# Optimization experiments

Hardware: AMD Instinct MI355X
Metric: run time of the kernel (lower is better)

## Reference

```python
import jax, jax.numpy as jnp
import numpy as np

TOLX = 1e-12
TOLFUN = 1e-06
MAXITER = 1000
ALPHA = 1e-4
MIN_LAMBDA = 0.1
MAX_LAMBDA = 0.5
MAX_STEPS = 10  # fixed unroll budget; Newton converges in < 10 iterations for this problem
BS, NY = 200000, 8


def setup_inputs():
    key = jax.random.key(0)
    k1, k2, k3 = jax.random.split(key, 3)
    y0 = jax.random.normal(k1, (BS, NY), dtype=jnp.float32)
    W = 0.1 * jax.random.normal(k2, (NY, NY), dtype=jnp.float32)
    V = 0.1 * jax.random.normal(k3, (NY, NY), dtype=jnp.float32)
    dt = jnp.asarray(0.1, dtype=jnp.float32)
    t = jnp.asarray(1.0, dtype=jnp.float32)
    return {"y0": y0, "dt": dt, "t": t, "W": W, "V": V}


def _safe_div(n, d, eps=1e-30):
    ok = jnp.abs(d) > eps
    return jnp.where(ok, n / jnp.where(ok, d, 1.0), 0.0)


def _solver(y0, dt, t, W, V):
    bs, ny = y0.shape
    one = jnp.float32(1.0)

    def delta_S(tt, y):
        # test ODE right-hand side g(t, y): mildly nonlinear, acts per-sample
        return jnp.tanh(y @ W) @ V - 0.1 * y + 0.01 * jnp.sin(tt)

    def err(y):  # implicit-Euler residual, (bs, ny)
        return (y - y0) / dt - delta_S(t, y)

    def _err_single(yb, y0b):
        return (yb - y0b) / dt - (jnp.tanh(yb @ W) @ V - 0.1 * yb + 0.01 * jnp.sin(t))

    def batched_jac(y):
        # (bs, ny, ny): d err_b / d y_b; matches torch batch-diagonal of autograd jacobian
        return jax.vmap(jax.jacfwd(_err_single), in_axes=(0, 0))(y, y0)

    F0 = err(y0)
    jac0 = batched_jac(y0)
    rn0 = jnp.max(jnp.abs(F0), axis=1)
    fobj0 = jnp.einsum('bi,bi->b', F0, F0)

    state0 = dict(y=y0, yold=y0, F=F0, dy=jnp.zeros_like(y0), jac=jac0,
                  resnorm=rn0, resnorm0=100.0 * rn0,
                  lam=one, lam1=one, lam2=jnp.float32(0.5),
                  fold=fobj0, f2=fobj0, slope=jnp.zeros((bs,), y0.dtype),
                  lam_min=jnp.float32(0.0), niter=jnp.int32(0), exitflag=jnp.int32(1))

    def body(s, _):
        active = (((jnp.max(s['resnorm']) > TOLFUN) | (s['lam'] < 1.0))
                  & (s['exitflag'] >= 0) & (s['niter'] <= MAXITER))

        # --- lam == 1: fresh Newton direction, slope, objective ---
        is_newton = s['lam'] == 1.0
        recompute = jnp.max(_safe_div(s['resnorm'], s['resnorm0'])) > 0.2
        fresh_jac = batched_jac(s['y'])
        jac = jnp.where(is_newton & recompute, fresh_jac, s['jac'])
        dy_n = -jnp.linalg.solve(jac, s['F'][..., None])[..., 0]  # lstsq on square == solve
        gvec = jnp.einsum('bi,bij->bj', s['F'], jac)
        slope_n = jnp.einsum('bj,bj->b', gvec, dy_n)
        fold_n = jnp.einsum('bi,bi->b', s['F'], s['F'])
        lam_min_n = _safe_div(jnp.float32(TOLX),
                              jnp.max(jnp.abs(dy_n) / jnp.maximum(jnp.abs(s['y']), 1.0)))

        dy = jnp.where(is_newton, dy_n, s['dy'])
        slope = jnp.where(is_newton, slope_n, s['slope'])
        fold = jnp.where(is_newton, fold_n, s['fold'])
        yold = jnp.where(is_newton, s['y'], s['yold'])
        lam_min = jnp.where(is_newton, lam_min_n, s['lam_min'])
        niter = jnp.where(is_newton, s['niter'] + 1, s['niter'])

        brk = s['lam'] < lam_min            # -> exitflag = 2, freeze state
        bad = ~jnp.all(jnp.isfinite(dy))    # -> exitflag = -1, freeze state

        # --- trial step + trust-region line search ---
        lam = s['lam']
        y_new = yold + dy * lam
        F_new = err(y_new)
        f_obj = jnp.einsum('bi,bi->b', F_new, F_new)
        lam1 = lam
        lam2, f2 = s['lam2'], s['f2']

        backtrack = jnp.any(f_obj > fold + ALPHA * lam * slope)
        # quadratic model (first backtrack)
        lam_quad = jnp.min(_safe_div(-slope / 2.0, f_obj - fold - slope))
        # cubic model (subsequent backtracks)
        A = _safe_div(one, lam1 - lam2)
        inv1 = _safe_div(one, lam1 * lam1)
        inv2 = _safe_div(one, lam2 * lam2)
        B = jnp.stack([jnp.stack([inv1, -inv2]), jnp.stack([-lam2 * inv1, lam1 * inv2])])
        C = jnp.stack([f_obj - fold - lam1 * slope, f2 - fold - lam2 * slope])  # (2, bs)
        ab = A * (B @ C)
        a, b = ab[0], ab[1]
        disc = b * b - 3.0 * a * slope
        sq = jnp.sqrt(jnp.maximum(disc, 0.0))
        lam_tmp = jnp.where(jnp.all(a == 0.0), _safe_div(-slope, 2.0 * b),
                   jnp.where(jnp.any(disc < 0.0), MAX_LAMBDA * lam1,
                    jnp.where(jnp.any(b <= 0.0), _safe_div(-b + sq, 3.0 * a),
                     _safe_div(-slope, b + sq))))
        lam_cubic = jnp.min(jnp.minimum(lam_tmp, MAX_LAMBDA * lam1))
        lam_bt = jnp.where(lam == 1.0, lam_quad, lam_cubic)
        nanf = ~jnp.all(jnp.isfinite(f_obj))
        lam_new = jnp.where(backtrack, lam_bt, jnp.where(nanf, MAX_LAMBDA * lam1, one))

        cont = lam_new < 1.0  # retry with smaller lambda next iteration (the `continue` path)
        lam2_new = jnp.where(cont, lam1, lam2)
        f2_new = jnp.where(cont, f_obj, f2)
        lam_new = jnp.where(cont, jnp.maximum(lam_new, MIN_LAMBDA * lam1), lam_new)
        resnorm_new = jnp.where(cont, s['resnorm'], jnp.max(jnp.abs(F_new), axis=1))
        resnorm0_new = jnp.where(cont, s['resnorm0'], s['resnorm'])

        upd = active & (~brk) & (~bad)
        exitflag = jnp.where(active & brk, jnp.int32(2),
                    jnp.where(active & (~brk) & bad, jnp.int32(-1), s['exitflag']))
        sel = lambda new, old: jnp.where(upd, new, old)

        ns = dict(y=sel(y_new, s['y']), yold=sel(yold, s['yold']), F=sel(F_new, s['F']),
                  dy=sel(dy, s['dy']), jac=sel(jac, s['jac']),
                  resnorm=sel(resnorm_new, s['resnorm']), resnorm0=sel(resnorm0_new, s['resnorm0']),
                  lam=sel(lam_new, s['lam']), lam1=sel(lam1, s['lam1']), lam2=sel(lam2_new, s['lam2']),
                  fold=sel(fold, s['fold']), f2=sel(f2_new, s['f2']), slope=sel(slope, s['slope']),
                  lam_min=sel(lam_min, s['lam_min']),
                  niter=jnp.where(active, niter, s['niter']), exitflag=exitflag)
        return ns, None

    sN, _ = jax.lax.scan(body, state0, None, length=MAX_STEPS)
    return sN['y'], sN['F'], sN['exitflag']


def reference(y0, dt, t, W, V):
    y, F, exitflag = _solver(y0, dt, t, W, V)
    return (y, F, exitflag)
```

## Files before the change

kernel.cpp:

```cpp
#include <hip/hip_runtime.h>
#include <hip/hip_cooperative_groups.h>

namespace cg = cooperative_groups;

#define BSZ 200000
#define NSTEPS 10
#define TOLFUN_C 1e-6f
#define ALPHA_C 1e-4f

#define CNTHR 256
#define CNBLK 512
#define CNT   (CNBLK*CNTHR)
#define SPT   2
#define SLOTS (CNTHR*SPT)

#define FNTHR 256
#define FNBLK ((BSZ + FNTHR - 1)/FNTHR)

#define OFF_Y     ((size_t)0)
#define OFF_YOLD  ((size_t)BSZ*8)
#define OFF_DY    ((size_t)BSZ*16)
#define OFF_SJ    ((size_t)BSZ*24)
#define OFF_FOLD  ((size_t)BSZ*32)
#define OFF_SLOPE ((size_t)BSZ*33)
#define OFF_RESN  ((size_t)BSZ*34)
#define OFF_F2    ((size_t)BSZ*35)
#define OFF_TFO   ((size_t)BSZ*36)
#define OFF_TRN   ((size_t)BSZ*37)
#define OFF_R     ((size_t)BSZ*38)

#define RSTRIDE 64
#define NSLOT   9
#define R_TOT   (2 + NSTEPS*NSLOT)
#define KEY_MAX_IDENT 0x007FFFFFu
#define KEY_MIN_IDENT 0xFF800000u

static __device__ __forceinline__ float nanmax2(float a, float b){
    return (__builtin_isnan(a) || __builtin_isnan(b)) ? __builtin_nanf("") : fmaxf(a, b);
}
static __device__ __forceinline__ float nanmin2(float a, float b){
    return (__builtin_isnan(a) || __builtin_isnan(b)) ? __builtin_nanf("") : fminf(a, b);
}
static __device__ __forceinline__ float safe_div(float n, float d){
    return (fabsf(d) > 1e-30f) ? (n / d) : 0.0f;
}
static __device__ __forceinline__ unsigned fkey(float x){
    unsigned u = __float_as_uint(x);
    return (u & 0x80000000u) ? ~u : (u | 0x80000000u);
}
static __device__ __forceinline__ float funkey(unsigned u){
    return (u & 0x80000000u) ? __uint_as_float(u & 0x7FFFFFFFu) : __uint_as_float(~u);
}
static __device__ __forceinline__ unsigned fkey_max(float x){
    if (__builtin_isnan(x)) x = __uint_as_float(0x7FC00000u);
    return fkey(x);
}
static __device__ __forceinline__ unsigned fkey_min(float x){
    if (__builtin_isnan(x)) x = __uint_as_float(0xFFC00000u);
    return fkey(x);
}
static __device__ __forceinline__ void ld8(const float* p, float* v){
    float4 a = ((const float4*)p)[0], b = ((const float4*)p)[1];
    v[0]=a.x; v[1]=a.y; v[2]=a.z; v[3]=a.w; v[4]=b.x; v[5]=b.y; v[6]=b.z; v[7]=b.w;
}
static __device__ __forceinline__ void st8(float* p, const float* v){
    float4 a, b;
    a.x=v[0]; a.y=v[1]; a.z=v[2]; a.w=v[3];
    b.x=v[4]; b.y=v[5]; b.z=v[6]; b.w=v[7];
    ((float4*)p)[0]=a; ((float4*)p)[1]=b;
}
static __device__ __forceinline__ unsigned ldslot(const unsigned* p){
    return __hip_atomic_load(p, __ATOMIC_RELAXED, __HIP_MEMORY_SCOPE_AGENT);
}
static __device__ __forceinline__ void stslot(unsigned* p, unsigned v){
    __hip_atomic_store(p, v, __ATOMIC_RELAXED, __HIP_MEMORY_SCOPE_AGENT);
}

static __device__ __forceinline__ void computeFz(
    const float* yv, const float* y0v, float dt, float c0,
    const float* sW, const float* sV, float* Fo, float* zo)
{
    float u[8];
    #pragma unroll
    for (int k=0;k<8;k++){
        float acc = 0.f;
        #pragma unroll
        for (int m=0;m<8;m++) acc += yv[m]*sW[m*8+k];
        u[k]=acc;
    }
    #pragma unroll
    for (int k=0;k<8;k++) zo[k] = tanhf(u[k]);
    #pragma unroll
    for (int i=0;i<8;i++){
        float tv = 0.f;
        #pragma unroll
        for (int k=0;k<8;k++) tv += zo[k]*sV[k*8+i];
        Fo[i] = (yv[i]-y0v[i])/dt - ((tv - 0.1f*yv[i]) + c0);
    }
}

static __device__ __forceinline__ void devInit2(const float* y0v,
    float* yold, float* dy, float* sj, float* F_out,
    float& fold_o, float& slope_o, float& resn_o, float& f2_o,
    float dt, float c0, const float* sW, const float* sV,
    float& rn_red, float& rat_red)
{
    #pragma unroll
    for (int i=0;i<8;i++){ yold[i]=y0v[i]; dy[i]=0.f; }
    float z[8];
    computeFz(y0v, y0v, dt, c0, sW, sV, F_out, z);
    #pragma unroll
    for (int k=0;k<8;k++) sj[k] = 1.0f - z[k]*z[k];
    float fold = 0.f;
    #pragma unroll
    for (int i=0;i<8;i++) fold += F_out[i]*F_out[i];
    float rn0 = fabsf(F_out[0]);
    #pragma unroll
    for (int i=1;i<8;i++) rn0 = nanmax2(rn0, fabsf(F_out[i]));
    fold_o=fold; slope_o=0.f; resn_o=rn0; f2_o=fold;
    rn_red  = nanmax2(rn_red, rn0);
    rat_red = nanmax2(rat_red, safe_div(rn0, 100.0f*rn0));
}

static __device__ __forceinline__ void devA4(const float* y_cur, const float* Fv,
    float* yold, float* dy, float* sj, float& fold_o, float& slope_o,
    float invdt, const float* sW, const float* sV,
    bool recompute, float& gml, bool& nf)
{
    if (recompute){
        float u[8];
        #pragma unroll
        for (int k=0;k<8;k++){
            float acc = 0.f;
            #pragma unroll
            for (int m=0;m<8;m++) acc += y_cur[m]*sW[m*8+k];
            u[k]=acc;
        }
        #pragma unroll
        for (int k=0;k<8;k++){ float z = tanhf(u[k]); sj[k] = 1.0f - z*z; }
    }
    const float c  = invdt + 0.1f;
    const float rc = 1.0f / c;
    float s[8], acc[8];
    #pragma unroll
    for (int i=0;i<8;i++){ s[i]=Fv[i]; acc[i]=Fv[i]; }
    for (int it=0; it<7; ++it){
        float w1[8];
        #pragma unroll
        for (int k=0;k<8;k++){
            float a = 0.f;
            #pragma unroll
            for (int j=0;j<8;j++) a += sW[j*8+k]*s[j];
            w1[k] = a*sj[k];
        }
        #pragma unroll
        for (int i=0;i<8;i++){
            float a = 0.f;
            #pragma unroll
            for (int k=0;k<8;k++) a += sV[k*8+i]*w1[k];
            s[i] = a*rc;
            acc[i] += s[i];
        }
    }
    #pragma unroll
    for (int i=0;i<8;i++) dy[i] = -(rc*acc[i]);
    float vf[8];
    #pragma unroll
    for (int k=0;k<8;k++){
        float a = 0.f;
        #pragma unroll
        for (int i=0;i<8;i++) a += sV[k*8+i]*Fv[i];
        vf[k] = a*sj[k];
    }
    float fold = 0.f, slope = 0.f;
    #pragma unroll
    for (int i=0;i<8;i++) fold += Fv[i]*Fv[i];
    #pragma unroll
    for (int j=0;j<8;j++){
        float a = 0.f;
        #pragma unroll
        for (int k=0;k<8;k++) a += sW[j*8+k]*vf[k];
        float gvj = c*Fv[j] - a;
        slope += gvj*dy[j];
    }
    #pragma unroll
    for (int i=0;i<8;i++){
        yold[i] = y_cur[i];
        float rr = fabsf(dy[i]) / nanmax2(fabsf(y_cur[i]), 1.0f);
        gml = nanmax2(gml, rr);
        nf = nf || !__builtin_isfinite(dy[i]);
    }
    fold_o = fold; slope_o = slope;
}

static __device__ __forceinline__ void devA2(const float* y_cur, const float* y0v,
    float* yold, float* dy, float* sj, float& fold_o, float& slope_o,
    float dt, float invdt, float c0, const float* sW, const float* sV,
    bool recompute, float& gml, bool& nf)
{
    float Fv[8], z[8];
    computeFz(y_cur, y0v, dt, c0, sW, sV, Fv, z);
    if (recompute){
        #pragma unroll
        for (int k=0;k<8;k++) sj[k] = 1.0f - z[k]*z[k];
    }
    devA4(y_cur, Fv, yold, dy, sj, fold_o, slope_o, invdt, sW, sV, false, gml, nf);
}

static __device__ __forceinline__ void devB2(const float* yold, const float* dy,
    const float* y0v, float foldv, float slopev, float resnv, float f2v,
    float dt, float c0, const float* sW, const float* sV, float lam, float lam2v,
    float* Ft, float& tfo_o, float& trn_o,
    bool& armijo, float& lq, bool& aNot0, bool& dN, bool& ble,
    float& mX, float& mZ, float& mW, bool& nanf, float& trnR, float& ratR)
{
    float yn[8];
    #pragma unroll
    for (int i=0;i<8;i++) yn[i] = yold[i] + dy[i]*lam;
    float z[8];
    computeFz(yn, y0v, dt, c0, sW, sV, Ft, z);
    float f_obj = 0.f;
    #pragma unroll
    for (int i=0;i<8;i++) f_obj += Ft[i]*Ft[i];
    float rn = fabsf(Ft[0]);
    #pragma unroll
    for (int i=1;i<8;i++) rn = nanmax2(rn, fabsf(Ft[i]));
    tfo_o = f_obj; trn_o = rn;
    armijo = armijo || (f_obj > (foldv + (ALPHA_C*lam)*slopev));
    lq = nanmin2(lq, safe_div((-slopev)*0.5f, (f_obj - foldv) - slopev));
    float lam1v = lam;
    float Af = safe_div(1.0f, lam1v - lam2v);
    float i1 = safe_div(1.0f, lam1v*lam1v);
    float i2 = safe_div(1.0f, lam2v*lam2v);
    float Cc0 = (f_obj - foldv) - lam1v*slopev;
    float Cc1 = (f2v   - foldv) - lam2v*slopev;
    float av = Af*(i1*Cc0 - i2*Cc1);
    float bv = Af*((-(lam2v*i1))*Cc0 + (lam1v*i2)*Cc1);
    float disc = bv*bv - (3.0f*av)*slopev;
    float dm = __builtin_isnan(disc) ? disc : fmaxf(disc, 0.0f);
    float sq = sqrtf(dm);
    aNot0 = aNot0 || (av != 0.0f);
    dN    = dN    || (disc < 0.0f);
    ble   = ble   || (bv <= 0.0f);
    mX = nanmin2(mX, safe_div(-slopev, 2.0f*bv));
    mZ = nanmin2(mZ, safe_div(-bv + sq, 3.0f*av));
    mW = nanmin2(mW, safe_div(-slopev, bv + sq));
    nanf = nanf || !__builtin_isfinite(f_obj);
    trnR = nanmax2(trnR, rn);
    ratR = nanmax2(ratR, safe_div(rn, resnv));
}

struct ScalarState {
    float lam, lam1, lam2, lam_min, maxrn, ratmax;
    int   niter, exitflag;
    bool  upd_prev, cont_prev;
};

static __device__ void advance(ScalarState& s, const unsigned* R, int j){
    const unsigned* r = R + (size_t)(2 + j*NSLOT)*RSTRIDE;
    unsigned v0 = ldslot(r + (size_t)0*RSTRIDE);
    unsigned v1 = ldslot(r + (size_t)1*RSTRIDE);
    unsigned v2 = ldslot(r + (size_t)2*RSTRIDE);
    unsigned v3 = ldslot(r + (size_t)3*RSTRIDE);
    unsigned v4 = ldslot(r + (size_t)4*RSTRIDE);
    unsigned v5 = ldslot(r + (size_t)5*RSTRIDE);
    unsigned v6 = ldslot(r + (size_t)6*RSTRIDE);
    unsigned v7 = ldslot(r + (size_t)7*RSTRIDE);
    unsigned v8 = ldslot(r + (size_t)8*RSTRIDE);
    bool active    = ((s.maxrn > TOLFUN_C) || (s.lam < 1.0f)) && (s.exitflag >= 0) && (s.niter <= 1000);
    bool is_newton = (s.lam == 1.0f);
    float lam_min_new = is_newton ? safe_div(1e-12f, funkey(v0)) : s.lam_min;
    bool brk = (s.lam < lam_min_new);
    bool bad = is_newton ? (v1 != 0u) : false;
    bool upd = active && !brk && !bad;
    int niter_new = active ? (is_newton ? s.niter + 1 : s.niter) : s.niter;
    int ef_new = s.exitflag;
    if (active && brk) ef_new = 2;
    else if (active && !brk && bad) ef_new = -1;
    bool cont = false;
    if (upd){
        float lam1c = s.lam;
        unsigned bm = v8;
        bool backtrack = (bm & 1u) != 0u;
        float lamq  = funkey(v2);
        bool allA0  = (bm & 2u) == 0u;
        bool anyDN  = (bm & 4u) != 0u;
        bool anyB0  = (bm & 8u) != 0u;
        float lam_tmp_min = allA0 ? funkey(v3)
                          : (anyDN ? (0.5f*lam1c)
                          : (anyB0 ? funkey(v4) : funkey(v5)));
        float lam_cubic = nanmin2(lam_tmp_min, 0.5f*lam1c);
        float lam_bt = (s.lam == 1.0f) ? lamq : lam_cubic;
        bool nanf = (bm & 16u) != 0u;
        float lam_new = backtrack ? lam_bt : (nanf ? 0.5f*lam1c : 1.0f);
        cont = (lam_new < 1.0f);
        float lam2_new = cont ? lam1c : s.lam2;
        if (cont) lam_new = nanmax2(lam_new, 0.1f*lam1c);
        float maxrn_new  = cont ? s.maxrn  : funkey(v6);
        float ratmax_new = cont ? s.ratmax : funkey(v7);
        s.lam = lam_new; s.lam1 = lam1c; s.lam2 = lam2_new;
        s.lam_min = lam_min_new; s.maxrn = maxrn_new; s.ratmax = ratmax_new;
    }
    s.niter = niter_new; s.exitflag = ef_new;
    s.upd_prev = upd; s.cont_prev = cont;
}

static __device__ ScalarState replayN(const unsigned* R, int n){
    ScalarState s;
    s.lam=1.0f; s.lam1=1.0f; s.lam2=0.5f; s.lam_min=0.0f;
    s.maxrn  = funkey(ldslot(&R[0]));
    s.ratmax = funkey(ldslot(&R[(size_t)1*RSTRIDE]));
    s.niter=0; s.exitflag=1; s.upd_prev=false; s.cont_prev=false;
    for (int j=0;j<n;++j) advance(s, R, j);
    return s;
}

__global__ __launch_bounds__(CNTHR, 2) void kFused(
    const float* __restrict__ y0g, const float* __restrict__ Wm, const float* __restrict__ Vm,
    const float* __restrict__ dtp, const float* __restrict__ tp,
    float* __restrict__ ws, float* __restrict__ out)
{
    cg::grid_group gridg = cg::this_grid();
    __shared__ float sW[64], sV[64];
    __shared__ float sSJ[8*SLOTS];
    __shared__ float sF0[8*SLOTS];
    __shared__ float sF1[8*SLOTS];
    __shared__ float redF[6][4];
    __shared__ unsigned redB[4];
    int t = threadIdx.x;
    if (t < 64) sW[t] = Wm[t];
    else if (t < 128) sV[t-64] = Vm[t-64];
    unsigned* R = (unsigned*)(ws + OFF_R);
    if (blockIdx.x == 0 && t < R_TOT){
        unsigned v;
        if (t < 2) v = KEY_MAX_IDENT;
        else {
            int off = (t - 2) % NSLOT;
            bool ismin = (off==2 || off==3 || off==4 || off==5);
            bool ismax = (off==0 || off==6 || off==7);
            v = ismin ? KEY_MIN_IDENT : (ismax ? KEY_MAX_IDENT : 0u);
        }
        stslot(&R[(size_t)t*RSTRIDE], v);
    }
    __syncthreads();
    gridg.sync();

    int gtid = blockIdx.x*CNTHR + t;
    float dt = *dtp, invdt = 1.0f/dt, c0 = 0.01f*sinf(*tp);

    bool  valid[SPT];
    float yold[SPT][8], dyv[SPT][8];
    float foldv[SPT], slopev[SPT], resnv[SPT], f2v[SPT], tfov[SPT], trnv[SPT];
    float lamc = 0.0f;
    int   pcur = 0;

    float rn_red = -__builtin_inff(), rat_red = -__builtin_inff();
    #pragma unroll
    for (int q=0;q<SPT;q++){
        int sid = gtid + q*CNT;
        int slot = q*CNTHR + t;
        valid[q] = sid < BSZ;
        if (valid[q]){
            float y0v[8], sjl[8], Fl[8];
            ld8(y0g + (size_t)sid*8, y0v);
            devInit2(y0v, yold[q], dyv[q], sjl, Fl,
                     foldv[q], slopev[q], resnv[q], f2v[q],
                     dt, c0, sW, sV, rn_red, rat_red);
            #pragma unroll
            for (int i=0;i<8;i++){ sSJ[i*SLOTS + slot] = sjl[i]; sF0[i*SLOTS + slot] = Fl[i]; }
            tfov[q]=0.f; trnv[q]=0.f;
        } else {
            #pragma unroll
            for (int i=0;i<8;i++){ sSJ[i*SLOTS + slot]=0; sF0[i*SLOTS + slot]=0; sF1[i*SLOTS + slot]=0;
                                   yold[q][i]=0; dyv[q][i]=0; }
            foldv[q]=0; slopev[q]=0; resnv[q]=0; f2v[q]=0; tfov[q]=0; trnv[q]=0;
        }
    }
    #pragma unroll
    for (int o=32;o>=1;o>>=1){
        rn_red  = nanmax2(rn_red,  __shfl_xor(rn_red,  o, 64));
        rat_red = nanmax2(rat_red, __shfl_xor(rat_red, o, 64));
    }
    {
        int w = t >> 6;
        if ((t & 63) == 0){ redF[0][w] = rn_red; redF[1][w] = rat_red; }
        __syncthreads();
        if (t == 0){
            float a = redF[0][0];
            #pragma unroll
            for (int w2=1;w2<4;w2++) a = nanmax2(a, redF[0][w2]);
            atomicMax(&R[0], fkey_max(a));
        } else if (t == 1){
            float b = redF[1][0];
            #pragma unroll
            for (int w2=1;w2<4;w2++) b = nanmax2(b, redF[1][w2]);
            atomicMax(&R[(size_t)1*RSTRIDE], fkey_max(b));
        }
    }
    gridg.sync();

    ScalarState S;
    S.lam=1.0f; S.lam1=1.0f; S.lam2=0.5f; S.lam_min=0.0f;
    S.maxrn  = funkey(ldslot(&R[0]));
    S.ratmax = funkey(ldslot(&R[(size_t)1*RSTRIDE]));
    S.niter=0; S.exitflag=1; S.upd_prev=false; S.cont_prev=false;

    #pragma unroll 1
    for (int k=1; k<=NSTEPS; ++k){
        if (S.upd_prev){
            lamc = S.lam1;
            pcur ^= 1;
            #pragma unroll
            for (int q=0;q<SPT;q++){
                if (!valid[q]) continue;
                if (S.cont_prev) f2v[q]  = tfov[q];
                else             resnv[q] = trnv[q];
            }
        }
        float* sFcur  = pcur ? sF1 : sF0;
        float* sFpend = pcur ? sF0 : sF1;
        bool active    = ((S.maxrn > TOLFUN_C) || (S.lam < 1.0f)) && (S.exitflag >= 0) && (S.niter <= 1000);
        bool is_newton = (S.lam == 1.0f);
        unsigned* r = R + (size_t)(2 + (k-1)*NSLOT)*RSTRIDE;

        if (active && is_newton){
            bool recompute = (S.ratmax > 0.2f);
            float gml = -__builtin_inff(); bool nf = false;
            #pragma unroll
            for (int q=0;q<SPT;q++){
                if (!valid[q]) continue;
                int slot = q*CNTHR + t;
                float y_cur[8], sjl[8], Fl[8];
                #pragma unroll
                for (int i=0;i<8;i++){
                    y_cur[i] = yold[q][i] + dyv[q][i]*lamc;
                    sjl[i]   = sSJ[i*SLOTS + slot];
                    Fl[i]    = sFcur[i*SLOTS + slot];
                }
                devA4(y_cur, Fl, yold[q], dyv[q], sjl, foldv[q], slopev[q],
                      invdt, sW, sV, recompute, gml, nf);
                if (recompute){
                    #pragma unroll
                    for (int i=0;i<8;i++) sSJ[i*SLOTS + slot] = sjl[i];
                }
            }
            lamc = 0.0f;
            #pragma unroll
            for (int o=32;o>=1;o>>=1) gml = nanmax2(gml, __shfl_xor(gml, o, 64));
            unsigned long long anym = __ballot(nf ? 1 : 0);
            int w = t >> 6;
            if ((t & 63) == 0){ redF[0][w] = gml; redB[w] = anym ? 1u : 0u; }
            __syncthreads();
            if (t == 0){
                float v = redF[0][0];
                #pragma unroll
                for (int w2=1;w2<4;w2++) v = nanmax2(v, redF[0][w2]);
                atomicMax(&r[0], fkey_max(v));
            } else if (t == 1){
                unsigned bm = redB[0]|redB[1]|redB[2]|redB[3];
                if (bm) atomicOr(&r[(size_t)1*RSTRIDE], 1u);
            }
            __syncthreads();
        }

        if (active){
            float lam = S.lam, lam2v = S.lam2;
            bool armijo=false, aNot0=false, dN=false, ble=false, nanf=false;
            float lq=__builtin_inff(), mX=__builtin_inff(), mZ=__builtin_inff(), mW=__builtin_inff();
            float trnR=-__builtin_inff(), ratR=-__builtin_inff();
            #pragma unroll
            for (int q=0;q<SPT;q++){
                if (!valid[q]) continue;
                int sid = gtid + q*CNT;
                int slot = q*CNTHR + t;
                float y0v[8], Ftl[8];
                ld8(y0g + (size_t)sid*8, y0v);
                devB2(yold[q], dyv[q], y0v, foldv[q], slopev[q], resnv[q], f2v[q],
                      dt, c0, sW, sV, lam, lam2v, Ftl, tfov[q], trnv[q],
                      armijo, lq, aNot0, dN, ble, mX, mZ, mW, nanf, trnR, ratR);
                #pragma unroll
                for (int i=0;i<8;i++) sFpend[i*SLOTS + slot] = Ftl[i];
            }
            #pragma unroll
            for (int o=32;o>=1;o>>=1){
                lq   = nanmin2(lq,   __shfl_xor(lq,   o, 64));
                mX   = nanmin2(mX,   __shfl_xor(mX,   o, 64));
                mZ   = nanmin2(mZ,   __shfl_xor(mZ,   o, 64));
                mW   = nanmin2(mW,   __shfl_xor(mW,   o, 64));
                trnR = nanmax2(trnR, __shfl_xor(trnR, o, 64));
                ratR = nanmax2(ratR, __shfl_xor(ratR, o, 64));
            }
            unsigned long long bArm = __ballot(armijo ? 1 : 0);
            unsigned long long bA0  = __ballot(aNot0  ? 1 : 0);
            unsigned long long bDN  = __ballot(dN     ? 1 : 0);
            unsigned long long bB0  = __ballot(ble    ? 1 : 0);
            unsigned long long bNF  = __ballot(nanf   ? 1 : 0);
            int w = t >> 6;
            if ((t & 63) == 0){
                redF[0][w]=lq; redF[1][w]=mX; redF[2][w]=mZ; redF[3][w]=mW;
                redF[4][w]=trnR; redF[5][w]=ratR;
                redB[w] = (bArm?1u:0u) | (bA0?2u:0u) | (bDN?4u:0u) | (bB0?8u:0u) | (bNF?16u:0u);
            }
            __syncthreads();
            if (t < 6){
                float v = redF[t][0];
                bool ismin = (t < 4);
                #pragma unroll
                for (int w2=1;w2<4;w2++) v = ismin ? nanmin2(v, redF[t][w2]) : nanmax2(v, redF[t][w2]);
                unsigned* p = &r[(size_t)(t + 2)*RSTRIDE];
                if (ismin) atomicMin(p, fkey_min(v));
                else       atomicMax(p, fkey_max(v));
            } else if (t == 6){
                unsigned bm = redB[0]|redB[1]|redB[2]|redB[3];
                if (bm) atomicOr(&r[(size_t)8*RSTRIDE], bm);
            }
        }

        gridg.sync();
        advance(S, R, k-1);
    }

    if (S.upd_prev){ lamc = S.lam1; pcur ^= 1; }
    float* sFout = pcur ? sF1 : sF0;
    #pragma unroll
    for (int q=0;q<SPT;q++){
        if (!valid[q]) continue;
        int sid = gtid + q*CNT;
        int slot = q*CNTHR + t;
        float yf[8], Fl[8];
        #pragma unroll
        for (int i=0;i<8;i++){
            yf[i] = yold[q][i] + dyv[q][i]*lamc;
            Fl[i] = sFout[i*SLOTS + slot];
        }
        st8(out + (size_t)sid*8, yf);
        st8(out + (size_t)BSZ*8 + (size_t)sid*8, Fl);
    }
    if (gtid == 0) out[(size_t)BSZ*16] = (float)S.exitflag;
}

__global__ void kPre(unsigned* __restrict__ R){
    int i = threadIdx.x;
    if (i >= R_TOT) return;
    unsigned v;
    if (i < 2) v = KEY_MAX_IDENT;
    else {
        int off = (i - 2) % NSLOT;
        bool ismin = (off==2 || off==3 || off==4 || off==5);
        bool ismax = (off==0 || off==6 || off==7);
        v = ismin ? KEY_MIN_IDENT : (ismax ? KEY_MAX_IDENT : 0u);
    }
    R[(size_t)i*RSTRIDE] = v;
}

__global__ __launch_bounds__(FNTHR) void fInit(
    const float* __restrict__ y0g, const float* __restrict__ Wm, const float* __restrict__ Vm,
    const float* __restrict__ dtp, const float* __restrict__ tp, float* __restrict__ ws)
{
    __shared__ float sW[64], sV[64];
    __shared__ float red[2][4];
    int t = threadIdx.x;
    if (t < 64) sW[t] = Wm[t];
    else if (t < 128) sV[t-64] = Vm[t-64];
    __syncthreads();
    unsigned* R = (unsigned*)(ws + OFF_R);
    int tid = blockIdx.x*FNTHR + t;
    bool valid = tid < BSZ;
    float dt = *dtp, c0 = 0.01f*sinf(*tp);
    float rn_red = -__builtin_inff(), rat_red = -__builtin_inff();
    if (valid){
        float y0v[8], yo[8], dv[8], sj[8], Fv[8], fold, slope, resn, f2;
        ld8(y0g + (size_t)tid*8, y0v);
        devInit2(y0v, yo, dv, sj, Fv, fold, slope, resn, f2, dt, c0, sW, sV, rn_red, rat_red);
        st8(ws+OFF_Y   +(size_t)tid*8, y0v);
        st8(ws+OFF_YOLD+(size_t)tid*8, yo);
        st8(ws+OFF_DY  +(size_t)tid*8, dv);
        st8(ws+OFF_SJ  +(size_t)tid*8, sj);
        ws[OFF_FOLD+tid]=fold; ws[OFF_SLOPE+tid]=slope;
        ws[OFF_RESN+tid]=resn; ws[OFF_F2+tid]=f2;
        ws[OFF_TFO+tid]=0.f;   ws[OFF_TRN+tid]=0.f;
    }
    #pragma unroll
    for (int o=32;o>=1;o>>=1){
        rn_red  = nanmax2(rn_red,  __shfl_xor(rn_red,  o, 64));
        rat_red = nanmax2(rat_red, __shfl_xor(rat_red, o, 64));
    }
    int w = t >> 6;
    if ((t & 63) == 0){ red[0][w]=rn_red; red[1][w]=rat_red; }
    __syncthreads();
    if (t == 0){
        float a = red[0][0];
        for (int w2=1;w2<4;w2++) a = nanmax2(a, red[0][w2]);
        atomicMax(&R[0], fkey_max(a));
    } else if (t == 1){
        float b = red[1][0];
        for (int w2=1;w2<4;w2++) b = nanmax2(b, red[1][w2]);
        atomicMax(&R[(size_t)1*RSTRIDE], fkey_max(b));
    }
}

__global__ __launch_bounds__(FNTHR) void fStep(
    const float* __restrict__ y0g, const float* __restrict__ Wm, const float* __restrict__ Vm,
    const float* __restrict__ dtp, const float* __restrict__ tp,
    float* __restrict__ ws, int step)
{
    __shared__ float sW[64], sV[64];
    __shared__ float redF[6][4];
    __shared__ unsigned redB[4];
    int t = threadIdx.x;
    if (t < 64) sW[t] = Wm[t];
    else if (t < 128) sV[t-64] = Vm[t-64];
    __syncthreads();
    unsigned* R = (unsigned*)(ws + OFF_R);
    ScalarState S = replayN(R, step-1);
    bool active    = ((S.maxrn > TOLFUN_C) || (S.lam < 1.0f)) && (S.exitflag >= 0) && (S.niter <= 1000);
    bool is_newton = (S.lam == 1.0f);
    if (!S.upd_prev && !active) return;

    int tid = blockIdx.x*FNTHR + t;
    bool valid = tid < BSZ;
    float dt = *dtp, invdt = 1.0f/dt, c0 = 0.01f*sinf(*tp);
    unsigned* r = R + (size_t)(2 + (step-1)*NSLOT)*RSTRIDE;

    float y0v[8], yv[8], yo[8], dv[8], sj[8], fold=0, slope=0, resn=0, f2=0;
    if (valid){
        ld8(y0g + (size_t)tid*8, y0v);
        ld8(ws+OFF_Y   +(size_t)tid*8, yv);
        ld8(ws+OFF_YOLD+(size_t)tid*8, yo);
        ld8(ws+OFF_DY  +(size_t)tid*8, dv);
        ld8(ws+OFF_SJ  +(size_t)tid*8, sj);
        fold=ws[OFF_FOLD+tid]; slope=ws[OFF_SLOPE+tid];
        resn=ws[OFF_RESN+tid]; f2=ws[OFF_F2+tid];
        if (S.upd_prev){
            #pragma unroll
            for (int i=0;i<8;i++) yv[i] = yo[i] + dv[i]*S.lam1;
            st8(ws+OFF_Y+(size_t)tid*8, yv);
            if (S.cont_prev){ f2 = ws[OFF_TFO+tid];  ws[OFF_F2+tid]   = f2; }
            else            { resn = ws[OFF_TRN+tid]; ws[OFF_RESN+tid] = resn; }
        }
    }
    if (!active) return;

    if (is_newton){
        bool recompute = (S.ratmax > 0.2f);
        float gml = -__builtin_inff(); bool nf = false;
        if (valid){
            devA2(yv, y0v, yo, dv, sj, fold, slope, dt, invdt, c0, sW, sV, recompute, gml, nf);
            st8(ws+OFF_YOLD+(size_t)tid*8, yo);
            st8(ws+OFF_DY  +(size_t)tid*8, dv);
            if (recompute) st8(ws+OFF_SJ+(size_t)tid*8, sj);
            ws[OFF_FOLD+tid]  = fold;
            ws[OFF_SLOPE+tid] = slope;
        }
        #pragma unroll
        for (int o=32;o>=1;o>>=1) gml = nanmax2(gml, __shfl_xor(gml, o, 64));
        unsigned long long anym = __ballot(nf ? 1 : 0);
        int w = t >> 6;
        if ((t & 63) == 0){ redF[0][w] = gml; redB[w] = anym ? 1u : 0u; }
        __syncthreads();
        if (t == 0){
            float v = redF[0][0];
            for (int w2=1;w2<4;w2++) v = nanmax2(v, redF[0][w2]);
            atomicMax(&r[0], fkey_max(v));
        } else if (t == 1){
            unsigned bm = redB[0]|redB[1]|redB[2]|redB[3];
            if (bm) atomicOr(&r[(size_t)1*RSTRIDE], 1u);
        }
        __syncthreads();
    }

    {
        float lam = S.lam, lam2v = S.lam2;
        bool armijo=false, aNot0=false, dN=false, ble=false, nanf=false;
        float lq=__builtin_inff(), mX=__builtin_inff(), mZ=__builtin_inff(), mW=__builtin_inff();
        float trnR=-__builtin_inff(), ratR=-__builtin_inff();
        if (valid){
            float tfo, trn, Ftl[8];
            devB2(yo, dv, y0v, fold, slope, resn, f2, dt, c0, sW, sV, lam, lam2v,
                  Ftl, tfo, trn, armijo, lq, aNot0, dN, ble, mX, mZ, mW, nanf, trnR, ratR);
            ws[OFF_TFO+tid] = tfo;
            ws[OFF_TRN+tid] = trn;
        }
        #pragma unroll
        for (int o=32;o>=1;o>>=1){
            lq   = nanmin2(lq,   __shfl_xor(lq,   o, 64));
            mX   = nanmin2(mX,   __shfl_xor(mX,   o, 64));
            mZ   = nanmin2(mZ,   __shfl_xor(mZ,   o, 64));
            mW   = nanmin2(mW,   __shfl_xor(mW,   o, 64));
            trnR = nanmax2(trnR, __shfl_xor(trnR, o, 64));
            ratR = nanmax2(ratR, __shfl_xor(ratR, o, 64));
        }
        unsigned long long bArm = __ballot(armijo ? 1 : 0);
        unsigned long long bA0  = __ballot(aNot0  ? 1 : 0);
        unsigned long long bDN  = __ballot(dN     ? 1 : 0);
        unsigned long long bB0  = __ballot(ble    ? 1 : 0);
        unsigned long long bNF  = __ballot(nanf   ? 1 : 0);
        int w = t >> 6;
        if ((t & 63) == 0){
            redF[0][w]=lq; redF[1][w]=mX; redF[2][w]=mZ; redF[3][w]=mW;
            redF[4][w]=trnR; redF[5][w]=ratR;
            redB[w] = (bArm?1u:0u) | (bA0?2u:0u) | (bDN?4u:0u) | (bB0?8u:0u) | (bNF?16u:0u);
        }
        __syncthreads();
        if (t < 6){
            float v = redF[t][0];
            bool ismin = (t < 4);
            for (int w2=1;w2<4;w2++) v = ismin ? nanmin2(v, redF[t][w2]) : nanmax2(v, redF[t][w2]);
            unsigned* p = &r[(size_t)(t + 2)*RSTRIDE];
            if (ismin) atomicMin(p, fkey_min(v));
            else       atomicMax(p, fkey_max(v));
        } else if (t == 6){
            unsigned bm = redB[0]|redB[1]|redB[2]|redB[3];
            if (bm) atomicOr(&r[(size_t)8*RSTRIDE], bm);
        }
    }
}

__global__ __launch_bounds__(FNTHR) void fOut(
    const float* __restrict__ y0g, const float* __restrict__ Wm, const float* __restrict__ Vm,
    const float* __restrict__ dtp, const float* __restrict__ tp,
    const float* __restrict__ ws, float* __restrict__ out)
{
    __shared__ float sW[64], sV[64];
    int t = threadIdx.x;
    if (t < 64) sW[t] = Wm[t];
    else if (t < 128) sV[t-64] = Vm[t-64];
    __syncthreads();
    const unsigned* R = (const unsigned*)(ws + OFF_R);
    ScalarState S = replayN(R, NSTEPS);
    int tid = blockIdx.x*FNTHR + t;
    float dt = *dtp, c0 = 0.01f*sinf(*tp);
    if (tid < BSZ){
        float y0v[8], yv[8];
        ld8(y0g + (size_t)tid*8, y0v);
        ld8(ws+OFF_Y+(size_t)tid*8, yv);
        if (S.upd_prev){
            float yo[8], dv[8];
            ld8(ws+OFF_YOLD+(size_t)tid*8, yo);
            ld8(ws+OFF_DY  +(size_t)tid*8, dv);
            #pragma unroll
            for (int i=0;i<8;i++) yv[i] = yo[i] + dv[i]*S.lam1;
        }
        st8(out + (size_t)tid*8, yv);
        float Fv[8], z[8];
        computeFz(yv, y0v, dt, c0, sW, sV, Fv, z);
        st8(out + (size_t)BSZ*8 + (size_t)tid*8, Fv);
    }
    if (blockIdx.x == 0 && t == 0) out[(size_t)BSZ*16] = (float)S.exitflag;
}

extern "C" void kernel_launch(void* const* d_in, const int* in_sizes, int n_in,
                              void* d_out, int out_size, void* d_ws, size_t ws_size,
                              hipStream_t stream)
{
    const float* y0g = (const float*)d_in[0];
    const float* dtp = (const float*)d_in[1];
    const float* tp  = (const float*)d_in[2];
    const float* Wm  = (const float*)d_in[3];
    const float* Vm  = (const float*)d_in[4];
    float* ws   = (float*)d_ws;
    float* outp = (float*)d_out;

    int occ = 0;
    hipError_t qrc = hipOccupancyMaxActiveBlocksPerMultiprocessor(
        &occ, (const void*)kFused, CNTHR, 0);
    bool try_coop = (qrc == hipSuccess && occ * 256 >= CNBLK);

    hipError_t rc = hipErrorUnknown;
    if (try_coop){
        void* args[] = {(void*)&y0g, (void*)&Wm, (void*)&Vm, (void*)&dtp, (void*)&tp,
                        (void*)&ws, (void*)&outp};
        rc = hipLaunchCooperativeKernel((const void*)kFused, dim3(CNBLK), dim3(CNTHR),
                                        args, 0, stream);
    }
    if (rc != hipSuccess){
        hipLaunchKernelGGL(kPre, dim3(1), dim3(128), 0, stream, (unsigned*)(ws + OFF_R));
        hipLaunchKernelGGL(fInit, dim3(FNBLK), dim3(FNTHR), 0, stream, y0g, Wm, Vm, dtp, tp, ws);
        for (int s = 1; s <= NSTEPS; ++s)
            hipLaunchKernelGGL(fStep, dim3(FNBLK), dim3(FNTHR), 0, stream, y0g, Wm, Vm, dtp, tp, ws, s);
        hipLaunchKernelGGL(fOut, dim3(FNBLK), dim3(FNTHR), 0, stream, y0g, Wm, Vm, dtp, tp, ws, outp);
    }
}
```

Before: 444.7 us.

## Replace cooperative grid sync with custom atomic barrier and move per-sample state to LDS

```diff
diff --git a/kernel.cpp b/kernel.cpp
--- a/kernel.cpp
+++ b/kernel.cpp
@@ -1,7 +1,4 @@
 #include <hip/hip_runtime.h>
-#include <hip/hip_cooperative_groups.h>
-
-namespace cg = cooperative_groups;
 
 #define BSZ 200000
 #define NSTEPS 10
@@ -14,21 +11,6 @@
 #define SPT   2
 #define SLOTS (CNTHR*SPT)
 
-#define FNTHR 256
-#define FNBLK ((BSZ + FNTHR - 1)/FNTHR)
-
-#define OFF_Y     ((size_t)0)
-#define OFF_YOLD  ((size_t)BSZ*8)
-#define OFF_DY    ((size_t)BSZ*16)
-#define OFF_SJ    ((size_t)BSZ*24)
-#define OFF_FOLD  ((size_t)BSZ*32)
-#define OFF_SLOPE ((size_t)BSZ*33)
-#define OFF_RESN  ((size_t)BSZ*34)
-#define OFF_F2    ((size_t)BSZ*35)
-#define OFF_TFO   ((size_t)BSZ*36)
-#define OFF_TRN   ((size_t)BSZ*37)
-#define OFF_R     ((size_t)BSZ*38)
-
 #define RSTRIDE 64
 #define NSLOT   9
 #define R_TOT   (2 + NSTEPS*NSLOT)
@@ -76,6 +58,17 @@
     __hip_atomic_store(p, v, __ATOMIC_RELAXED, __HIP_MEMORY_SCOPE_AGENT);
 }
 
+static __device__ __forceinline__ void gridBar(unsigned* bar, unsigned target, int t){
+    __syncthreads();
+    if (t == 0){
+        __hip_atomic_fetch_add(bar, 1u, __ATOMIC_RELEASE, __HIP_MEMORY_SCOPE_AGENT);
+        while (__hip_atomic_load(bar, __ATOMIC_ACQUIRE, __HIP_MEMORY_SCOPE_AGENT) < target){
+            __builtin_amdgcn_s_sleep(2);
+        }
+    }
+    __syncthreads();
+}
+
 static __device__ __forceinline__ void computeFz(
     const float* yv, const float* y0v, float dt, float c0,
     const float* sW, const float* sV, float* Fo, float* zo)
@@ -99,46 +92,10 @@
     }
 }
 
-static __device__ __forceinline__ void devInit2(const float* y0v,
-    float* yold, float* dy, float* sj, float* F_out,
-    float& fold_o, float& slope_o, float& resn_o, float& f2_o,
-    float dt, float c0, const float* sW, const float* sV,
-    float& rn_red, float& rat_red)
+static __device__ __forceinline__ void neumann(const float* Fv, const float* sj,
+    float invdt, const float* sW, const float* sV,
+    float* dy, float& fold_o, float& slope_o)
 {
-    #pragma unroll
-    for (int i=0;i<8;i++){ yold[i]=y0v[i]; dy[i]=0.f; }
-    float z[8];
-    computeFz(y0v, y0v, dt, c0, sW, sV, F_out, z);
-    #pragma unroll
-    for (int k=0;k<8;k++) sj[k] = 1.0f - z[k]*z[k];
-    float fold = 0.f;
-    #pragma unroll
-    for (int i=0;i<8;i++) fold += F_out[i]*F_out[i];
-    float rn0 = fabsf(F_out[0]);
-    #pragma unroll
-    for (int i=1;i<8;i++) rn0 = nanmax2(rn0, fabsf(F_out[i]));
-    fold_o=fold; slope_o=0.f; resn_o=rn0; f2_o=fold;
-    rn_red  = nanmax2(rn_red, rn0);
-    rat_red = nanmax2(rat_red, safe_div(rn0, 100.0f*rn0));
-}
-
-static __device__ __forceinline__ void devA4(const float* y_cur, const float* Fv,
-    float* yold, float* dy, float* sj, float& fold_o, float& slope_o,
-    float invdt, const float* sW, const float* sV,
-    bool recompute, float& gml, bool& nf)
-{
-    if (recompute){
-        float u[8];
-        #pragma unroll
-        for (int k=0;k<8;k++){
-            float acc = 0.f;
-            #pragma unroll
-            for (int m=0;m<8;m++) acc += y_cur[m]*sW[m*8+k];
-            u[k]=acc;
-        }
-        #pragma unroll
-        for (int k=0;k<8;k++){ float z = tanhf(u[k]); sj[k] = 1.0f - z*z; }
-    }
     const float c  = invdt + 0.1f;
     const float rc = 1.0f / c;
     float s[8], acc[8];
@@ -183,71 +140,7 @@
         float gvj = c*Fv[j] - a;
         slope += gvj*dy[j];
     }
-    #pragma unroll
-    for (int i=0;i<8;i++){
-        yold[i] = y_cur[i];
-        float rr = fabsf(dy[i]) / nanmax2(fabsf(y_cur[i]), 1.0f);
-        gml = nanmax2(gml, rr);
-        nf = nf || !__builtin_isfinite(dy[i]);
-    }
     fold_o = fold; slope_o = slope;
-}
-
-static __device__ __forceinline__ void devA2(const float* y_cur, const float* y0v,
-    float* yold, float* dy, float* sj, float& fold_o, float& slope_o,
-    float dt, float invdt, float c0, const float* sW, const float* sV,
-    bool recompute, float& gml, bool& nf)
-{
-    float Fv[8], z[8];
-    computeFz(y_cur, y0v, dt, c0, sW, sV, Fv, z);
-    if (recompute){
-        #pragma unroll
-        for (int k=0;k<8;k++) sj[k] = 1.0f - z[k]*z[k];
-    }
-    devA4(y_cur, Fv, yold, dy, sj, fold_o, slope_o, invdt, sW, sV, false, gml, nf);
-}
-
-static __device__ __forceinline__ void devB2(const float* yold, const float* dy,
-    const float* y0v, float foldv, float slopev, float resnv, float f2v,
-    float dt, float c0, const float* sW, const float* sV, float lam, float lam2v,
-    float* Ft, float& tfo_o, float& trn_o,
-    bool& armijo, float& lq, bool& aNot0, bool& dN, bool& ble,
-    float& mX, float& mZ, float& mW, bool& nanf, float& trnR, float& ratR)
-{
-    float yn[8];
-    #pragma unroll
-    for (int i=0;i<8;i++) yn[i] = yold[i] + dy[i]*lam;
-    float z[8];
-    computeFz(yn, y0v, dt, c0, sW, sV, Ft, z);
-    float f_obj = 0.f;
-    #pragma unroll
-    for (int i=0;i<8;i++) f_obj += Ft[i]*Ft[i];
-    float rn = fabsf(Ft[0]);
-    #pragma unroll
-    for (int i=1;i<8;i++) rn = nanmax2(rn, fabsf(Ft[i]));
-    tfo_o = f_obj; trn_o = rn;
-    armijo = armijo || (f_obj > (foldv + (ALPHA_C*lam)*slopev));
-    lq = nanmin2(lq, safe_div((-slopev)*0.5f, (f_obj - foldv) - slopev));
-    float lam1v = lam;
-    float Af = safe_div(1.0f, lam1v - lam2v);
-    float i1 = safe_div(1.0f, lam1v*lam1v);
-    float i2 = safe_div(1.0f, lam2v*lam2v);
-    float Cc0 = (f_obj - foldv) - lam1v*slopev;
-    float Cc1 = (f2v   - foldv) - lam2v*slopev;
-    float av = Af*(i1*Cc0 - i2*Cc1);
-    float bv = Af*((-(lam2v*i1))*Cc0 + (lam1v*i2)*Cc1);
-    float disc = bv*bv - (3.0f*av)*slopev;
-    float dm = __builtin_isnan(disc) ? disc : fmaxf(disc, 0.0f);
-    float sq = sqrtf(dm);
-    aNot0 = aNot0 || (av != 0.0f);
-    dN    = dN    || (disc < 0.0f);
-    ble   = ble   || (bv <= 0.0f);
-    mX = nanmin2(mX, safe_div(-slopev, 2.0f*bv));
-    mZ = nanmin2(mZ, safe_div(-bv + sq, 3.0f*av));
-    mW = nanmin2(mW, safe_div(-slopev, bv + sq));
-    nanf = nanf || !__builtin_isfinite(f_obj);
-    trnR = nanmax2(trnR, rn);
-    ratR = nanmax2(ratR, safe_div(rn, resnv));
 }
 
 struct ScalarState {
@@ -305,54 +198,49 @@
     s.upd_prev = upd; s.cont_prev = cont;
 }
 
-static __device__ ScalarState replayN(const unsigned* R, int n){
-    ScalarState s;
-    s.lam=1.0f; s.lam1=1.0f; s.lam2=0.5f; s.lam_min=0.0f;
-    s.maxrn  = funkey(ldslot(&R[0]));
-    s.ratmax = funkey(ldslot(&R[(size_t)1*RSTRIDE]));
-    s.niter=0; s.exitflag=1; s.upd_prev=false; s.cont_prev=false;
-    for (int j=0;j<n;++j) advance(s, R, j);
-    return s;
-}
-
-__global__ __launch_bounds__(CNTHR, 2) void kFused(
+__global__ void kPre(unsigned* __restrict__ R){
+    int i = threadIdx.x;
+    if (i < R_TOT){
+        unsigned v;
+        if (i < 2) v = KEY_MAX_IDENT;
+        else {
+            int off = (i - 2) % NSLOT;
+            bool ismin = (off==2 || off==3 || off==4 || off==5);
+            bool ismax = (off==0 || off==6 || off==7);
+            v = ismin ? KEY_MIN_IDENT : (ismax ? KEY_MAX_IDENT : 0u);
+        }
+        R[(size_t)i*RSTRIDE] = v;
+    } else if (i == R_TOT){
+        stslot(&R[(size_t)R_TOT*RSTRIDE], 0u);
+    }
+}
+
+__global__ __launch_bounds__(CNTHR, 2) void kMain(
     const float* __restrict__ y0g, const float* __restrict__ Wm, const float* __restrict__ Vm,
     const float* __restrict__ dtp, const float* __restrict__ tp,
     float* __restrict__ ws, float* __restrict__ out)
 {
-    cg::grid_group gridg = cg::this_grid();
     __shared__ float sW[64], sV[64];
+    __shared__ float sYOLD[8*SLOTS];
     __shared__ float sSJ[8*SLOTS];
-    __shared__ float sF0[8*SLOTS];
-    __shared__ float sF1[8*SLOTS];
+    __shared__ float sSC[6*SLOTS];
     __shared__ float redF[6][4];
     __shared__ unsigned redB[4];
     int t = threadIdx.x;
     if (t < 64) sW[t] = Wm[t];
     else if (t < 128) sV[t-64] = Vm[t-64];
-    unsigned* R = (unsigned*)(ws + OFF_R);
-    if (blockIdx.x == 0 && t < R_TOT){
-        unsigned v;
-        if (t < 2) v = KEY_MAX_IDENT;
-        else {
-            int off = (t - 2) % NSLOT;
-            bool ismin = (off==2 || off==3 || off==4 || off==5);
-            bool ismax = (off==0 || off==6 || off==7);
-            v = ismin ? KEY_MIN_IDENT : (ismax ? KEY_MAX_IDENT : 0u);
-        }
-        stslot(&R[(size_t)t*RSTRIDE], v);
-    }
     __syncthreads();
-    gridg.sync();
+
+    unsigned* R = (unsigned*)ws;
+    unsigned* bar = R + (size_t)R_TOT*RSTRIDE;
+    unsigned bcnt = 0;
 
     int gtid = blockIdx.x*CNTHR + t;
     float dt = *dtp, invdt = 1.0f/dt, c0 = 0.01f*sinf(*tp);
 
     bool  valid[SPT];
-    float yold[SPT][8], dyv[SPT][8];
-    float foldv[SPT], slopev[SPT], resnv[SPT], f2v[SPT], tfov[SPT], trnv[SPT];
+    float dyv[SPT][8];
     float lamc = 0.0f;
-    int   pcur = 0;
 
     float rn_red = -__builtin_inff(), rat_red = -__builtin_inff();
     #pragma unroll
@@ -361,19 +249,31 @@
         int slot = q*CNTHR + t;
         valid[q] = sid < BSZ;
         if (valid[q]){
-            float y0v[8], sjl[8], Fl[8];
+            float y0v[8], Fv[8], z[8];
             ld8(y0g + (size_t)sid*8, y0v);
-            devInit2(y0v, yold[q], dyv[q], sjl, Fl,
-                     foldv[q], slopev[q], resnv[q], f2v[q],
-                     dt, c0, sW, sV, rn_red, rat_red);
-            #pragma unroll
-            for (int i=0;i<8;i++){ sSJ[i*SLOTS + slot] = sjl[i]; sF0[i*SLOTS + slot] = Fl[i]; }
-            tfov[q]=0.f; trnv[q]=0.f;
+            computeFz(y0v, y0v, dt, c0, sW, sV, Fv, z);
+            float fold = 0.f;
+            #pragma unroll
+            for (int i=0;i<8;i++) fold += Fv[i]*Fv[i];
+            float rn0 = fabsf(Fv[0]);
+            #pragma unroll
+            for (int i=1;i<8;i++) rn0 = nanmax2(rn0, fabsf(Fv[i]));
+            #pragma unroll
+            for (int i=0;i<8;i++){
+                sYOLD[i*SLOTS + slot] = y0v[i];
+                sSJ[i*SLOTS + slot]   = 1.0f - z[i]*z[i];
+                dyv[q][i] = 0.f;
+            }
+            sSC[0*SLOTS+slot]=fold; sSC[1*SLOTS+slot]=0.f;
+            sSC[2*SLOTS+slot]=rn0;  sSC[3*SLOTS+slot]=fold;
+            sSC[4*SLOTS+slot]=0.f;  sSC[5*SLOTS+slot]=0.f;
+            rn_red  = nanmax2(rn_red, rn0);
+            rat_red = nanmax2(rat_red, safe_div(rn0, 100.0f*rn0));
         } else {
             #pragma unroll
-            for (int i=0;i<8;i++){ sSJ[i*SLOTS + slot]=0; sF0[i*SLOTS + slot]=0; sF1[i*SLOTS + slot]=0;
-                                   yold[q][i]=0; dyv[q][i]=0; }
-            foldv[q]=0; slopev[q]=0; resnv[q]=0; f2v[q]=0; tfov[q]=0; trnv[q]=0;
+            for (int i=0;i<8;i++){ sYOLD[i*SLOTS+slot]=0; sSJ[i*SLOTS+slot]=0; dyv[q][i]=0; }
+            #pragma unroll
+            for (int c=0;c<6;c++) sSC[c*SLOTS+slot]=0;
         }
     }
     #pragma unroll
@@ -397,7 +297,7 @@
             atomicMax(&R[(size_t)1*RSTRIDE], fkey_max(b));
         }
     }
-    gridg.sync();
+    bcnt++; gridBar(bar, (unsigned)CNBLK*bcnt, t);
 
     ScalarState S;
     S.lam=1.0f; S.lam1=1.0f; S.lam2=0.5f; S.lam_min=0.0f;
@@ -409,16 +309,14 @@
     for (int k=1; k<=NSTEPS; ++k){
         if (S.upd_prev){
             lamc = S.lam1;
-            pcur ^= 1;
             #pragma unroll
             for (int q=0;q<SPT;q++){
                 if (!valid[q]) continue;
-                if (S.cont_prev) f2v[q]  = tfov[q];
-                else             resnv[q] = trnv[q];
-            }
-        }
-        float* sFcur  = pcur ? sF1 : sF0;
-        float* sFpend = pcur ? sF0 : sF1;
+                int slot = q*CNTHR + t;
+                if (S.cont_prev) sSC[3*SLOTS+slot] = sSC[4*SLOTS+slot];
+                else             sSC[2*SLOTS+slot] = sSC[5*SLOTS+slot];
+            }
+        }
         bool active    = ((S.maxrn > TOLFUN_C) || (S.lam < 1.0f)) && (S.exitflag >= 0) && (S.niter <= 1000);
         bool is_newton = (S.lam == 1.0f);
         unsigned* r = R + (size_t)(2 + (k-1)*NSLOT)*RSTRIDE;
@@ -429,19 +327,32 @@
             #pragma unroll
             for (int q=0;q<SPT;q++){
                 if (!valid[q]) continue;
+                int sid = gtid + q*CNT;
                 int slot = q*CNTHR + t;
-                float y_cur[8], sjl[8], Fl[8];
-                #pragma unroll
-                for (int i=0;i<8;i++){
-                    y_cur[i] = yold[q][i] + dyv[q][i]*lamc;
-                    sjl[i]   = sSJ[i*SLOTS + slot];
-                    Fl[i]    = sFcur[i*SLOTS + slot];
-                }
-                devA4(y_cur, Fl, yold[q], dyv[q], sjl, foldv[q], slopev[q],
-                      invdt, sW, sV, recompute, gml, nf);
+                float y_cur[8], y0v[8], Fv[8], z[8], sjl[8];
+                #pragma unroll
+                for (int i=0;i<8;i++) y_cur[i] = sYOLD[i*SLOTS+slot] + dyv[q][i]*lamc;
+                ld8(y0g + (size_t)sid*8, y0v);
+                computeFz(y_cur, y0v, dt, c0, sW, sV, Fv, z);
                 if (recompute){
                     #pragma unroll
-                    for (int i=0;i<8;i++) sSJ[i*SLOTS + slot] = sjl[i];
+                    for (int i=0;i<8;i++){ sjl[i] = 1.0f - z[i]*z[i]; sSJ[i*SLOTS+slot] = sjl[i]; }
+                } else {
+                    #pragma unroll
+                    for (int i=0;i<8;i++) sjl[i] = sSJ[i*SLOTS+slot];
+                }
+                #pragma unroll
+                for (int i=0;i<8;i++) sYOLD[i*SLOTS+slot] = y_cur[i];
+                float fold, slope;
+                neumann(Fv, sjl, invdt, sW, sV, dyv[q], fold, slope);
+                sSC[0*SLOTS+slot] = fold;
+                sSC[1*SLOTS+slot] = slope;
+                #pragma unroll
+                for (int i=0;i<8;i++){
+                    float yc = sYOLD[i*SLOTS+slot];
+                    float rr = fabsf(dyv[q][i]) / nanmax2(fabsf(yc), 1.0f);
+                    gml = nanmax2(gml, rr);
+                    nf = nf || !__builtin_isfinite(dyv[q][i]);
                 }
             }
             lamc = 0.0f;
@@ -473,13 +384,45 @@
                 if (!valid[q]) continue;
                 int sid = gtid + q*CNT;
                 int slot = q*CNTHR + t;
-                float y0v[8], Ftl[8];
+                float yn[8], y0v[8], Ft[8], z[8];
+                #pragma unroll
+                for (int i=0;i<8;i++) yn[i] = sYOLD[i*SLOTS+slot] + dyv[q][i]*lam;
                 ld8(y0g + (size_t)sid*8, y0v);
-                devB2(yold[q], dyv[q], y0v, foldv[q], slopev[q], resnv[q], f2v[q],
-                      dt, c0, sW, sV, lam, lam2v, Ftl, tfov[q], trnv[q],
-                      armijo, lq, aNot0, dN, ble, mX, mZ, mW, nanf, trnR, ratR);
-                #pragma unroll
-                for (int i=0;i<8;i++) sFpend[i*SLOTS + slot] = Ftl[i];
+                computeFz(yn, y0v, dt, c0, sW, sV, Ft, z);
+                float f_obj = 0.f;
+                #pragma unroll
+                for (int i=0;i<8;i++) f_obj += Ft[i]*Ft[i];
+                float rn = fabsf(Ft[0]);
+                #pragma unroll
+                for (int i=1;i<8;i++) rn = nanmax2(rn, fabsf(Ft[i]));
+                sSC[4*SLOTS+slot] = f_obj;
+                sSC[5*SLOTS+slot] = rn;
+                float foldv  = sSC[0*SLOTS+slot];
+                float slopev = sSC[1*SLOTS+slot];
+                float resnv  = sSC[2*SLOTS+slot];
+                float f2v    = sSC[3*SLOTS+slot];
+                armijo = armijo || (f_obj > (foldv + (ALPHA_C*lam)*slopev));
+                lq = nanmin2(lq, safe_div((-slopev)*0.5f, (f_obj - foldv) - slopev));
+                float lam1v = lam;
+                float Af = safe_div(1.0f, lam1v - lam2v);
+                float i1 = safe_div(1.0f, lam1v*lam1v);
+                float i2 = safe_div(1.0f, lam2v*lam2v);
+                float Cc0 = (f_obj - foldv) - lam1v*slopev;
+                float Cc1 = (f2v   - foldv) - lam2v*slopev;
+                float av = Af*(i1*Cc0 - i2*Cc1);
+                float bv = Af*((-(lam2v*i1))*Cc0 + (lam1v*i2)*Cc1);
+                float disc = bv*bv - (3.0f*av)*slopev;
+                float dm = __builtin_isnan(disc) ? disc : fmaxf(disc, 0.0f);
+                float sq = sqrtf(dm);
+                aNot0 = aNot0 || (av != 0.0f);
+                dN    = dN    || (disc < 0.0f);
+                ble   = ble   || (bv <= 0.0f);
+                mX = nanmin2(mX, safe_div(-slopev, 2.0f*bv));
+                mZ = nanmin2(mZ, safe_div(-bv + sq, 3.0f*av));
+                mW = nanmin2(mW, safe_div(-slopev, bv + sq));
+                nanf = nanf || !__builtin_isfinite(f_obj);
+                trnR = nanmax2(trnR, rn);
+                ratR = nanmax2(ratR, safe_div(rn, resnv));
             }
             #pragma unroll
             for (int o=32;o>=1;o>>=1){
@@ -516,237 +459,25 @@
             }
         }
 
-        gridg.sync();
+        bcnt++; gridBar(bar, (unsigned)CNBLK*bcnt, t);
         advance(S, R, k-1);
     }
 
-    if (S.upd_prev){ lamc = S.lam1; pcur ^= 1; }
-    float* sFout = pcur ? sF1 : sF0;
+    if (S.upd_prev) lamc = S.lam1;
     #pragma unroll
     for (int q=0;q<SPT;q++){
         if (!valid[q]) continue;
         int sid = gtid + q*CNT;
         int slot = q*CNTHR + t;
-        float yf[8], Fl[8];
-        #pragma unroll
-        for (int i=0;i<8;i++){
-            yf[i] = yold[q][i] + dyv[q][i]*lamc;
-            Fl[i] = sFout[i*SLOTS + slot];
-        }
+        float yf[8], y0v[8], Fv[8], z[8];
+        #pragma unroll
+        for (int i=0;i<8;i++) yf[i] = sYOLD[i*SLOTS+slot] + dyv[q][i]*lamc;
+        ld8(y0g + (size_t)sid*8, y0v);
         st8(out + (size_t)sid*8, yf);
-        st8(out + (size_t)BSZ*8 + (size_t)sid*8, Fl);
+        computeFz(yf, y0v, dt, c0, sW, sV, Fv, z);
+        st8(out + (size_t)BSZ*8 + (size_t)sid*8, Fv);
     }
     if (gtid == 0) out[(size_t)BSZ*16] = (float)S.exitflag;
-}
-
-__global__ void kPre(unsigned* __restrict__ R){
-    int i = threadIdx.x;
-    if (i >= R_TOT) return;
-    unsigned v;
-    if (i < 2) v = KEY_MAX_IDENT;
-    else {
-        int off = (i - 2) % NSLOT;
-        bool ismin = (off==2 || off==3 || off==4 || off==5);
-        bool ismax = (off==0 || off==6 || off==7);
-        v = ismin ? KEY_MIN_IDENT : (ismax ? KEY_MAX_IDENT : 0u);
-    }
-    R[(size_t)i*RSTRIDE] = v;
-}
-
-__global__ __launch_bounds__(FNTHR) void fInit(
-    const float* __restrict__ y0g, const float* __restrict__ Wm, const float* __restrict__ Vm,
-    const float* __restrict__ dtp, const float* __restrict__ tp, float* __restrict__ ws)
-{
-    __shared__ float sW[64], sV[64];
-    __shared__ float red[2][4];
-    int t = threadIdx.x;
-    if (t < 64) sW[t] = Wm[t];
-    else if (t < 128) sV[t-64] = Vm[t-64];
-    __syncthreads();
-    unsigned* R = (unsigned*)(ws + OFF_R);
-    int tid = blockIdx.x*FNTHR + t;
-    bool valid = tid < BSZ;
-    float dt = *dtp, c0 = 0.01f*sinf(*tp);
-    float rn_red = -__builtin_inff(), rat_red = -__builtin_inff();
-    if (valid){
-        float y0v[8], yo[8], dv[8], sj[8], Fv[8], fold, slope, resn, f2;
-        ld8(y0g + (size_t)tid*8, y0v);
-        devInit2(y0v, yo, dv, sj, Fv, fold, slope, resn, f2, dt, c0, sW, sV, rn_red, rat_red);
-        st8(ws+OFF_Y   +(size_t)tid*8, y0v);
-        st8(ws+OFF_YOLD+(size_t)tid*8, yo);
-        st8(ws+OFF_DY  +(size_t)tid*8, dv);
-        st8(ws+OFF_SJ  +(size_t)tid*8, sj);
-        ws[OFF_FOLD+tid]=fold; ws[OFF_SLOPE+tid]=slope;
-        ws[OFF_RESN+tid]=resn; ws[OFF_F2+tid]=f2;
-        ws[OFF_TFO+tid]=0.f;   ws[OFF_TRN+tid]=0.f;
-    }
-    #pragma unroll
-    for (int o=32;o>=1;o>>=1){
-        rn_red  = nanmax2(rn_red,  __shfl_xor(rn_red,  o, 64));
-        rat_red = nanmax2(rat_red, __shfl_xor(rat_red, o, 64));
-    }
-    int w = t >> 6;
-    if ((t & 63) == 0){ red[0][w]=rn_red; red[1][w]=rat_red; }
-    __syncthreads();
-    if (t == 0){
-        float a = red[0][0];
-        for (int w2=1;w2<4;w2++) a = nanmax2(a, red[0][w2]);
-        atomicMax(&R[0], fkey_max(a));
-    } else if (t == 1){
-        float b = red[1][0];
-        for (int w2=1;w2<4;w2++) b = nanmax2(b, red[1][w2]);
-        atomicMax(&R[(size_t)1*RSTRIDE], fkey_max(b));
-    }
-}
-
-__global__ __launch_bounds__(FNTHR) void fStep(
-    const float* __restrict__ y0g, const float* __restrict__ Wm, const float* __restrict__ Vm,
-    const float* __restrict__ dtp, const float* __restrict__ tp,
-    float* __restrict__ ws, int step)
-{
-    __shared__ float sW[64], sV[64];
-    __shared__ float redF[6][4];
-    __shared__ unsigned redB[4];
-    int t = threadIdx.x;
-    if (t < 64) sW[t] = Wm[t];
-    else if (t < 128) sV[t-64] = Vm[t-64];
-    __syncthreads();
-    unsigned* R = (unsigned*)(ws + OFF_R);
-    ScalarState S = replayN(R, step-1);
-    bool active    = ((S.maxrn > TOLFUN_C) || (S.lam < 1.0f)) && (S.exitflag >= 0) && (S.niter <= 1000);
-    bool is_newton = (S.lam == 1.0f);
-    if (!S.upd_prev && !active) return;
-
-    int tid = blockIdx.x*FNTHR + t;
-    bool valid = tid < BSZ;
-    float dt = *dtp, invdt = 1.0f/dt, c0 = 0.01f*sinf(*tp);
-    unsigned* r = R + (size_t)(2 + (step-1)*NSLOT)*RSTRIDE;
-
-    float y0v[8], yv[8], yo[8], dv[8], sj[8], fold=0, slope=0, resn=0, f2=0;
-    if (valid){
-        ld8(y0g + (size_t)tid*8, y0v);
-        ld8(ws+OFF_Y   +(size_t)tid*8, yv);
-        ld8(ws+OFF_YOLD+(size_t)tid*8, yo);
-        ld8(ws+OFF_DY  +(size_t)tid*8, dv);
-        ld8(ws+OFF_SJ  +(size_t)tid*8, sj);
-        fold=ws[OFF_FOLD+tid]; slope=ws[OFF_SLOPE+tid];
-        resn=ws[OFF_RESN+tid]; f2=ws[OFF_F2+tid];
-        if (S.upd_prev){
-            #pragma unroll
-            for (int i=0;i<8;i++) yv[i] = yo[i] + dv[i]*S.lam1;
-            st8(ws+OFF_Y+(size_t)tid*8, yv);
-            if (S.cont_prev){ f2 = ws[OFF_TFO+tid];  ws[OFF_F2+tid]   = f2; }
-            else            { resn = ws[OFF_TRN+tid]; ws[OFF_RESN+tid] = resn; }
-        }
-    }
-    if (!active) return;
-
-    if (is_newton){
-        bool recompute = (S.ratmax > 0.2f);
-        float gml = -__builtin_inff(); bool nf = false;
-        if (valid){
-            devA2(yv, y0v, yo, dv, sj, fold, slope, dt, invdt, c0, sW, sV, recompute, gml, nf);
-            st8(ws+OFF_YOLD+(size_t)tid*8, yo);
-            st8(ws+OFF_DY  +(size_t)tid*8, dv);
-            if (recompute) st8(ws+OFF_SJ+(size_t)tid*8, sj);
-            ws[OFF_FOLD+tid]  = fold;
-            ws[OFF_SLOPE+tid] = slope;
-        }
-        #pragma unroll
-        for (int o=32;o>=1;o>>=1) gml = nanmax2(gml, __shfl_xor(gml, o, 64));
-        unsigned long long anym = __ballot(nf ? 1 : 0);
-        int w = t >> 6;
-        if ((t & 63) == 0){ redF[0][w] = gml; redB[w] = anym ? 1u : 0u; }
-        __syncthreads();
-        if (t == 0){
-            float v = redF[0][0];
-            for (int w2=1;w2<4;w2++) v = nanmax2(v, redF[0][w2]);
-            atomicMax(&r[0], fkey_max(v));
-        } else if (t == 1){
-            unsigned bm = redB[0]|redB[1]|redB[2]|redB[3];
-            if (bm) atomicOr(&r[(size_t)1*RSTRIDE], 1u);
-        }
-        __syncthreads();
-    }
-
-    {
-        float lam = S.lam, lam2v = S.lam2;
-        bool armijo=false, aNot0=false, dN=false, ble=false, nanf=false;
-        float lq=__builtin_inff(), mX=__builtin_inff(), mZ=__builtin_inff(), mW=__builtin_inff();
-        float trnR=-__builtin_inff(), ratR=-__builtin_inff();
-        if (valid){
-            float tfo, trn, Ftl[8];
-            devB2(yo, dv, y0v, fold, slope, resn, f2, dt, c0, sW, sV, lam, lam2v,
-                  Ftl, tfo, trn, armijo, lq, aNot0, dN, ble, mX, mZ, mW, nanf, trnR, ratR);
-            ws[OFF_TFO+tid] = tfo;
-            ws[OFF_TRN+tid] = trn;
-        }
-        #pragma unroll
-        for (int o=32;o>=1;o>>=1){
-            lq   = nanmin2(lq,   __shfl_xor(lq,   o, 64));
-            mX   = nanmin2(mX,   __shfl_xor(mX,   o, 64));
-            mZ   = nanmin2(mZ,   __shfl_xor(mZ,   o, 64));
-            mW   = nanmin2(mW,   __shfl_xor(mW,   o, 64));
-            trnR = nanmax2(trnR, __shfl_xor(trnR, o, 64));
-            ratR = nanmax2(ratR, __shfl_xor(ratR, o, 64));
-        }
-        unsigned long long bArm = __ballot(armijo ? 1 : 0);
-        unsigned long long bA0  = __ballot(aNot0  ? 1 : 0);
-        unsigned long long bDN  = __ballot(dN     ? 1 : 0);
-        unsigned long long bB0  = __ballot(ble    ? 1 : 0);
-        unsigned long long bNF  = __ballot(nanf   ? 1 : 0);
-        int w = t >> 6;
-        if ((t & 63) == 0){
-            redF[0][w]=lq; redF[1][w]=mX; redF[2][w]=mZ; redF[3][w]=mW;
-            redF[4][w]=trnR; redF[5][w]=ratR;
-            redB[w] = (bArm?1u:0u) | (bA0?2u:0u) | (bDN?4u:0u) | (bB0?8u:0u) | (bNF?16u:0u);
-        }
-        __syncthreads();
-        if (t < 6){
-            float v = redF[t][0];
-            bool ismin = (t < 4);
-            for (int w2=1;w2<4;w2++) v = ismin ? nanmin2(v, redF[t][w2]) : nanmax2(v, redF[t][w2]);
-            unsigned* p = &r[(size_t)(t + 2)*RSTRIDE];
-            if (ismin) atomicMin(p, fkey_min(v));
-            else       atomicMax(p, fkey_max(v));
-        } else if (t == 6){
-            unsigned bm = redB[0]|redB[1]|redB[2]|redB[3];
-            if (bm) atomicOr(&r[(size_t)8*RSTRIDE], bm);
-        }
-    }
-}
-
-__global__ __launch_bounds__(FNTHR) void fOut(
-    const float* __restrict__ y0g, const float* __restrict__ Wm, const float* __restrict__ Vm,
-    const float* __restrict__ dtp, const float* __restrict__ tp,
-    const float* __restrict__ ws, float* __restrict__ out)
-{
-    __shared__ float sW[64], sV[64];
-    int t = threadIdx.x;
-    if (t < 64) sW[t] = Wm[t];
-    else if (t < 128) sV[t-64] = Vm[t-64];
-    __syncthreads();
-    const unsigned* R = (const unsigned*)(ws + OFF_R);
-    ScalarState S = replayN(R, NSTEPS);
-    int tid = blockIdx.x*FNTHR + t;
-    float dt = *dtp, c0 = 0.01f*sinf(*tp);
-    if (tid < BSZ){
-        float y0v[8], yv[8];
-        ld8(y0g + (size_t)tid*8, y0v);
-        ld8(ws+OFF_Y+(size_t)tid*8, yv);
-        if (S.upd_prev){
-            float yo[8], dv[8];
-            ld8(ws+OFF_YOLD+(size_t)tid*8, yo);
-            ld8(ws+OFF_DY  +(size_t)tid*8, dv);
-            #pragma unroll
-            for (int i=0;i<8;i++) yv[i] = yo[i] + dv[i]*S.lam1;
-        }
-        st8(out + (size_t)tid*8, yv);
-        float Fv[8], z[8];
-        computeFz(yv, y0v, dt, c0, sW, sV, Fv, z);
-        st8(out + (size_t)BSZ*8 + (size_t)tid*8, Fv);
-    }
-    if (blockIdx.x == 0 && t == 0) out[(size_t)BSZ*16] = (float)S.exitflag;
 }
 
 extern "C" void kernel_launch(void* const* d_in, const int* in_sizes, int n_in,
@@ -761,23 +492,7 @@
     float* ws   = (float*)d_ws;
     float* outp = (float*)d_out;
 
-    int occ = 0;
-    hipError_t qrc = hipOccupancyMaxActiveBlocksPerMultiprocessor(
-        &occ, (const void*)kFused, CNTHR, 0);
-    bool try_coop = (qrc == hipSuccess && occ * 256 >= CNBLK);
-
-    hipError_t rc = hipErrorUnknown;
-    if (try_coop){
-        void* args[] = {(void*)&y0g, (void*)&Wm, (void*)&Vm, (void*)&dtp, (void*)&tp,
-                        (void*)&ws, (void*)&outp};
-        rc = hipLaunchCooperativeKernel((const void*)kFused, dim3(CNBLK), dim3(CNTHR),
-                                        args, 0, stream);
-    }
-    if (rc != hipSuccess){
-        hipLaunchKernelGGL(kPre, dim3(1), dim3(128), 0, stream, (unsigned*)(ws + OFF_R));
-        hipLaunchKernelGGL(fInit, dim3(FNBLK), dim3(FNTHR), 0, stream, y0g, Wm, Vm, dtp, tp, ws);
-        for (int s = 1; s <= NSTEPS; ++s)
-            hipLaunchKernelGGL(fStep, dim3(FNBLK), dim3(FNTHR), 0, stream, y0g, Wm, Vm, dtp, tp, ws, s);
-        hipLaunchKernelGGL(fOut, dim3(FNBLK), dim3(FNTHR), 0, stream, y0g, Wm, Vm, dtp, tp, ws, outp);
-    }
-}
+    hipLaunchKernelGGL(kPre, dim3(1), dim3(128), 0, stream, (unsigned*)ws);
+    hipLaunchKernelGGL(kMain, dim3(CNBLK), dim3(CNTHR), 0, stream,
+                       y0g, Wm, Vm, dtp, tp, ws, outp);
+}
```

Result: slower. 666.5 us (+49.9%).
